# Optimization experiments

Measured on AMD Instinct MI355X. Metric: run time of the kernel, lower is better.

## Reference

```python
import jax, jax.numpy as jnp
import numpy as np

B, D, E, K = 65536, 1024, 8, 2

def setup_inputs() -> dict:
    key = jax.random.key(0)
    k1, k2, k3, k4, k5 = jax.random.split(key, 5)
    s = 1.0 / np.sqrt(D)
    return {
        "x": jax.random.normal(k1, (B, D), dtype=jnp.float32),
        "gate_w": jax.random.uniform(k2, (E, D), dtype=jnp.float32, minval=-s, maxval=s),
        "gate_b": jax.random.uniform(k3, (E,), dtype=jnp.float32, minval=-s, maxval=s),
        "expert_w": jax.random.uniform(k4, (E, D), dtype=jnp.float32, minval=-s, maxval=s),  # row e = weight of expert e's Linear(D,1)
        "expert_b": jax.random.uniform(k5, (E,), dtype=jnp.float32, minval=-s, maxval=s),
        "k": K,
    }

def reference(x, gate_w, gate_b, expert_w, expert_b, k):
    # gate: [B, E]
    gate_scores = jax.nn.softmax(x @ gate_w.T + gate_b, axis=1)
    E_ = gate_w.shape[0]
    if k < E_:
        topk_vals, topk_idx = jax.lax.top_k(gate_scores, k)  # [B, k]
        rows = jnp.arange(x.shape[0])[:, None]
        gate_scores = jnp.zeros_like(gate_scores).at[rows, topk_idx].set(topk_vals)
    # per-expert Linear(D,1) stacked: [B, E]
    expert_outputs = x @ expert_w.T + expert_b
    # weighted sum over experts -> [B, 1]
    moe_output = jnp.sum(gate_scores * expert_outputs, axis=1, keepdims=True)
    return moe_output
```

## Files before the change

### kernel.cpp

```cpp
#include <hip/hip_runtime.h>


#define BLOCK 512
#define WAVES_PB (BLOCK / 64)
#define ROWS_PER_WAVE 16
#define ROWS_PER_BLOCK (WAVES_PB * ROWS_PER_WAVE)
#define DD 1024
#define EE 8

__global__ __launch_bounds__(BLOCK, 4) void moe_gate_kernel(
    const float* __restrict__ x,
    const float* __restrict__ gate_w,
    const float* __restrict__ gate_b,
    const float* __restrict__ expert_w,
    const float* __restrict__ expert_b,
    const int* __restrict__ kp,
    float* __restrict__ out)
{
    __shared__ float wlds[2 * EE * DD];

    const int tid = threadIdx.x;

    {
        const float4* g4 = (const float4*)gate_w;
        const float4* e4 = (const float4*)expert_w;
        float4* w4 = (float4*)wlds;
#pragma unroll
        for (int i = 0; i < (EE * DD / 4) / BLOCK; ++i) {
            int idx = i * BLOCK + tid;
            w4[idx] = g4[idx];
            w4[EE * DD / 4 + idx] = e4[idx];
        }
    }
    __syncthreads();

    const int lane = tid & 63;
    const int wave = tid >> 6;
    const int g = lane >> 2;
    const int j = lane & 3;

    const int row = blockIdx.x * ROWS_PER_BLOCK + wave * ROWS_PER_WAVE + g;
    const float* xr = x + (size_t)row * DD + j * 4;

    const float* wg = wlds + j * 4;
    const float* we = wlds + EE * DD + j * 4;

    float acc[16];
#pragma unroll
    for (int i = 0; i < 16; ++i) acc[i] = 0.f;

    auto step = [&](int c, const float4& xv) {
        const int wc = c * 16;
#pragma unroll
        for (int e = 0; e < EE; ++e) {
            float4 w1 = *(const float4*)(wg + e * DD + wc);
            acc[e] = fmaf(xv.x, w1.x, acc[e]);
            acc[e] = fmaf(xv.y, w1.y, acc[e]);
            acc[e] = fmaf(xv.z, w1.z, acc[e]);
            acc[e] = fmaf(xv.w, w1.w, acc[e]);
            float4 w2 = *(const float4*)(we + e * DD + wc);
            acc[8 + e] = fmaf(xv.x, w2.x, acc[8 + e]);
            acc[8 + e] = fmaf(xv.y, w2.y, acc[8 + e]);
            acc[8 + e] = fmaf(xv.z, w2.z, acc[8 + e]);
            acc[8 + e] = fmaf(xv.w, w2.w, acc[8 + e]);
        }
    };

    float4 cur = *(const float4*)(xr);
#pragma unroll 1
    for (int c = 0; c < DD / 16 - 1; ++c) {
        float4 nxt = *(const float4*)(xr + (c + 1) * 16);
        step(c, cur);
        cur = nxt;
    }
    step(DD / 16 - 1, cur);

#pragma unroll
    for (int i = 0; i < 16; ++i) {
        acc[i] += __shfl_xor(acc[i], 1);
        acc[i] += __shfl_xor(acc[i], 2);
    }

    if (j == 0) {
        float gl[8], eo[8], p[8];
#pragma unroll
        for (int e = 0; e < EE; ++e) {
            gl[e] = acc[e] + gate_b[e];
            eo[e] = acc[8 + e] + expert_b[e];
        }
        float m = gl[0];
#pragma unroll
        for (int e = 1; e < EE; ++e) m = fmaxf(m, gl[e]);
        float Z = 0.f;
#pragma unroll
        for (int e = 0; e < EE; ++e) { p[e] = __expf(gl[e] - m); Z += p[e]; }

        const int k = *kp;
        float res = 0.f;
        if (k >= EE) {
#pragma unroll
            for (int e = 0; e < EE; ++e) res += p[e] * eo[e];
        } else {
            float pv[8];
#pragma unroll
            for (int e = 0; e < EE; ++e) pv[e] = p[e];
            for (int t = 0; t < k; ++t) {
                float bv = pv[0];
#pragma unroll
                for (int e = 1; e < EE; ++e) bv = fmaxf(bv, pv[e]);
                float sel = 0.f;
                bool found = false;
#pragma unroll
                for (int e = 0; e < EE; ++e) {
                    bool is = (!found) && (pv[e] == bv);
                    sel = is ? eo[e] : sel;
                    pv[e] = is ? -1.f : pv[e];
                    found = found || is;
                }
                res += bv * sel;
            }
        }
        out[row] = res / Z;
    }
}

extern "C" void kernel_launch(void* const* d_in, const int* in_sizes, int n_in,
                              void* d_out, int out_size, void* d_ws, size_t ws_size,
                              hipStream_t stream) {
    const float* x  = (const float*)d_in[0];
    const float* gw = (const float*)d_in[1];
    const float* gb = (const float*)d_in[2];
    const float* ew = (const float*)d_in[3];
    const float* eb = (const float*)d_in[4];
    const int*   kp = (const int*)d_in[5];
    float* out = (float*)d_out;

    const int B = out_size;
    dim3 grid(B / ROWS_PER_BLOCK), block(BLOCK);
    moe_gate_kernel<<<grid, block, 0, stream>>>(x, gw, gb, ew, eb, kp, out);
}
```

Measured before the change: 55.92 us.

## Process two rows per lane group to reuse LDS weight loads

Each group of 8 lanes now computes two rows instead of 4 lanes computing one, so each float4 weight read from LDS feeds two rows' FMAs. This halves LDS traffic per FLOP, which was likely the bottleneck in the inner loop, and widens x loads per row to 8 lanes × 16 bytes. It doubles accumulator registers (32 per thread), adds one more shuffle stage, and reads two rows 4 KB apart per lane group, which may hurt occupancy or coalescing.

```diff
diff --git a/kernel.cpp b/kernel.cpp
--- a/kernel.cpp
+++ b/kernel.cpp
@@ -2,11 +2,10 @@
 
 
 #define BLOCK 512
-#define WAVES_PB (BLOCK / 64)
-#define ROWS_PER_WAVE 16
-#define ROWS_PER_BLOCK (WAVES_PB * ROWS_PER_WAVE)
 #define DD 1024
 #define EE 8
+#define ROWS_PER_WAVE 16
+#define ROWS_PER_BLOCK ((BLOCK / 64) * ROWS_PER_WAVE)
 
 __global__ __launch_bounds__(BLOCK, 4) void moe_gate_kernel(
     const float* __restrict__ x,
@@ -36,91 +35,100 @@
 
     const int lane = tid & 63;
     const int wave = tid >> 6;
-    const int g = lane >> 2;
-    const int j = lane & 3;
+    const int s = lane >> 3;
+    const int j = lane & 7;
 
-    const int row = blockIdx.x * ROWS_PER_BLOCK + wave * ROWS_PER_WAVE + g;
-    const float* xr = x + (size_t)row * DD + j * 4;
+    const int row0 = blockIdx.x * ROWS_PER_BLOCK + wave * ROWS_PER_WAVE + 2 * s;
+    const float* xr0 = x + (size_t)row0 * DD + j * 4;
+    const float* xr1 = xr0 + DD;
 
-    const float* wg = wlds + j * 4;
-    const float* we = wlds + EE * DD + j * 4;
+    const float* wb = wlds + j * 4;
 
-    float acc[16];
+    float acc0[16], acc1[16];
 #pragma unroll
-    for (int i = 0; i < 16; ++i) acc[i] = 0.f;
+    for (int i = 0; i < 16; ++i) { acc0[i] = 0.f; acc1[i] = 0.f; }
 
-    auto step = [&](int c, const float4& xv) {
-        const int wc = c * 16;
+    auto step = [&](int c, const float4& x0, const float4& x1) {
+        const int wc = c * 32;
 #pragma unroll
-        for (int e = 0; e < EE; ++e) {
-            float4 w1 = *(const float4*)(wg + e * DD + wc);
-            acc[e] = fmaf(xv.x, w1.x, acc[e]);
-            acc[e] = fmaf(xv.y, w1.y, acc[e]);
-            acc[e] = fmaf(xv.z, w1.z, acc[e]);
-            acc[e] = fmaf(xv.w, w1.w, acc[e]);
-            float4 w2 = *(const float4*)(we + e * DD + wc);
-            acc[8 + e] = fmaf(xv.x, w2.x, acc[8 + e]);
-            acc[8 + e] = fmaf(xv.y, w2.y, acc[8 + e]);
-            acc[8 + e] = fmaf(xv.z, w2.z, acc[8 + e]);
-            acc[8 + e] = fmaf(xv.w, w2.w, acc[8 + e]);
+        for (int o = 0; o < 16; ++o) {
+            float4 w = *(const float4*)(wb + o * DD + wc);
+            acc0[o] = fmaf(x0.x, w.x, acc0[o]);
+            acc1[o] = fmaf(x1.x, w.x, acc1[o]);
+            acc0[o] = fmaf(x0.y, w.y, acc0[o]);
+            acc1[o] = fmaf(x1.y, w.y, acc1[o]);
+            acc0[o] = fmaf(x0.z, w.z, acc0[o]);
+            acc1[o] = fmaf(x1.z, w.z, acc1[o]);
+            acc0[o] = fmaf(x0.w, w.w, acc0[o]);
+            acc1[o] = fmaf(x1.w, w.w, acc1[o]);
         }
     };
 
-    float4 cur = *(const float4*)(xr);
+    float4 a0 = *(const float4*)(xr0);
+    float4 a1 = *(const float4*)(xr1);
 #pragma unroll 1
-    for (int c = 0; c < DD / 16 - 1; ++c) {
-        float4 nxt = *(const float4*)(xr + (c + 1) * 16);
-        step(c, cur);
-        cur = nxt;
+    for (int c = 0; c < DD / 32 - 1; ++c) {
+        float4 b0 = *(const float4*)(xr0 + (c + 1) * 32);
+        float4 b1 = *(const float4*)(xr1 + (c + 1) * 32);
+        step(c, a0, a1);
+        a0 = b0; a1 = b1;
     }
-    step(DD / 16 - 1, cur);
+    step(DD / 32 - 1, a0, a1);
 
 #pragma unroll
     for (int i = 0; i < 16; ++i) {
-        acc[i] += __shfl_xor(acc[i], 1);
-        acc[i] += __shfl_xor(acc[i], 2);
+        acc0[i] += __shfl_xor(acc0[i], 1);
+        acc1[i] += __shfl_xor(acc1[i], 1);
+        acc0[i] += __shfl_xor(acc0[i], 2);
+        acc1[i] += __shfl_xor(acc1[i], 2);
+        acc0[i] += __shfl_xor(acc0[i], 4);
+        acc1[i] += __shfl_xor(acc1[i], 4);
     }
 
     if (j == 0) {
-        float gl[8], eo[8], p[8];
+        const int k = *kp;
 #pragma unroll
-        for (int e = 0; e < EE; ++e) {
-            gl[e] = acc[e] + gate_b[e];
-            eo[e] = acc[8 + e] + expert_b[e];
+        for (int r = 0; r < 2; ++r) {
+            const float* acc = r ? acc1 : acc0;
+            float gl[8], eo[8], p[8];
+#pragma unroll
+            for (int e = 0; e < EE; ++e) {
+                gl[e] = acc[e] + gate_b[e];
+                eo[e] = acc[8 + e] + expert_b[e];
+            }
+            float m = gl[0];
+#pragma unroll
+            for (int e = 1; e < EE; ++e) m = fmaxf(m, gl[e]);
+            float Z = 0.f;
+#pragma unroll
+            for (int e = 0; e < EE; ++e) { p[e] = __expf(gl[e] - m); Z += p[e]; }
+
+            float res = 0.f;
+            if (k >= EE) {
+#pragma unroll
+                for (int e = 0; e < EE; ++e) res += p[e] * eo[e];
+            } else {
+                float pv[8];
+#pragma unroll
+                for (int e = 0; e < EE; ++e) pv[e] = p[e];
+                for (int t = 0; t < k; ++t) {
+                    float bv = pv[0];
+#pragma unroll
+                    for (int e = 1; e < EE; ++e) bv = fmaxf(bv, pv[e]);
+                    float sel = 0.f;
+                    bool found = false;
+#pragma unroll
+                    for (int e = 0; e < EE; ++e) {
+                        bool is = (!found) && (pv[e] == bv);
+                        sel = is ? eo[e] : sel;
+                        pv[e] = is ? -1.f : pv[e];
+                        found = found || is;
+                    }
+                    res += bv * sel;
+                }
+            }
+            out[row0 + r] = res / Z;
         }
-        float m = gl[0];
-#pragma unroll
-        for (int e = 1; e < EE; ++e) m = fmaxf(m, gl[e]);
-        float Z = 0.f;
-#pragma unroll
-        for (int e = 0; e < EE; ++e) { p[e] = __expf(gl[e] - m); Z += p[e]; }
-
-        const int k = *kp;
-        float res = 0.f;
-        if (k >= EE) {
-#pragma unroll
-            for (int e = 0; e < EE; ++e) res += p[e] * eo[e];
-        } else {
-            float pv[8];
-#pragma unroll
-            for (int e = 0; e < EE; ++e) pv[e] = p[e];
-            for (int t = 0; t < k; ++t) {
-                float bv = pv[0];
-#pragma unroll
-                for (int e = 1; e < EE; ++e) bv = fmaxf(bv, pv[e]);
-                float sel = 0.f;
-                bool found = false;
-#pragma unroll
-                for (int e = 0; e < EE; ++e) {
-                    bool is = (!found) && (pv[e] == bv);
-                    sel = is ? eo[e] : sel;
-                    pv[e] = is ? -1.f : pv[e];
-                    found = found || is;
-                }
-                res += bv * sel;
-            }
-        }
-        out[row] = res / Z;
     }
 }
 
```

Result: faster. 50.11 us (-10.4%).
